# Optimization experiments

Measured on AMD Instinct MI355X. Metric: run time of the kernel, lower is better.

## Reference

```python
import jax, jax.numpy as jnp
import numpy as np

EPS_LN = 1e-5

def _layernorm(x, g, b):
    mu = jnp.mean(x, axis=-1, keepdims=True)
    var = jnp.mean((x - mu) ** 2, axis=-1, keepdims=True)
    return (x - mu) * jax.lax.rsqrt(var + EPS_LN) * g + b

def _act_quant_ste(x):
    # clip_val uses detached stats -> stop_gradient
    clip_val = jax.lax.stop_gradient(
        jnp.clip(jnp.mean(jnp.abs(x), axis=-1, keepdims=True), 1e-8, None)) * 2.5
    scale = clip_val / 127.0
    x_scaled = x / scale
    x_clip = jnp.clip(x_scaled, -127.0, 127.0)
    x_q = x_scaled + jax.lax.stop_gradient(jnp.round(x_clip) - x_scaled)
    return x_q * scale

def _weight_quant_ste(w):
    scale = jax.lax.stop_gradient(jnp.clip(jnp.mean(jnp.abs(w)), 1e-8, None))
    w_norm = w / scale
    w_clip = jnp.clip(w_norm, -1.0, 1.0)
    w_q = w_norm + jax.lax.stop_gradient(jnp.round(w_clip) - w_norm)
    return w_q * scale

def _bitlinear(x, w, g, b):
    # w: [out, in]; x: [B,T,in]
    x_q = _act_quant_ste(_layernorm(x, g, b))
    w_q = _weight_quant_ste(w)
    return jnp.einsum('btd,hd->bth', x_q, w_q)

def setup_inputs() -> dict:
    D, H = 2048, 2048 * 4
    B, T = 4, 2048
    key = jax.random.key(0)
    ks = jax.random.split(key, 4)
    std = 0.02
    return {
        'x': jax.random.normal(ks[0], (B, T, D), dtype=jnp.float32),
        'mu_k': jnp.zeros((1, 1, D), jnp.float32),
        'mu_r': jnp.zeros((1, 1, D), jnp.float32),
        'wk': jax.random.normal(ks[1], (H, D), jnp.float32) * std,
        'gk': jnp.ones((D,), jnp.float32), 'bk': jnp.zeros((D,), jnp.float32),
        'wr': jax.random.normal(ks[2], (D, D), jnp.float32) * std,
        'gr': jnp.ones((D,), jnp.float32), 'br': jnp.zeros((D,), jnp.float32),
        'wv': jax.random.normal(ks[3], (D, H), jnp.float32) * std,
        'gv': jnp.ones((H,), jnp.float32), 'bv': jnp.zeros((H,), jnp.float32),
    }

def reference(x, mu_k, mu_r, wk, gk, bk, wr, gr, br, wv, gv, bv):
    B, T, C = x.shape
    prev = jnp.zeros((B, 1, C), dtype=x.dtype)  # state=None path
    x_prev = jnp.concatenate([prev, x[:, :-1, :]], axis=1)  # token shift
    dx = x_prev - x
    k_act = jax.nn.relu(_bitlinear(x + dx * mu_k, wk, gk, bk)) ** 2  # [B,T,H]
    rgate = jax.nn.sigmoid(_bitlinear(x + dx * mu_r, wr, gr, br))    # [B,T,D]
    out = rgate * _bitlinear(k_act, wv, gv, bv)                      # [B,T,D]
    return out, jax.lax.stop_gradient(x[:, -1:, :])
```

## Files before the change

### kernel.cpp

```cpp
#include <hip/hip_runtime.h>

#define T_LEN 2048
#define B_SZ  4
#define D_DIM 2048
#define H_DIM 8192
#define BT    (B_SZ * T_LEN)

typedef float f32x4 __attribute__((ext_vector_type(4)));
typedef int   i32x4v __attribute__((ext_vector_type(4)));
typedef int   i32x16v __attribute__((ext_vector_type(16)));
typedef unsigned short ushort8 __attribute__((ext_vector_type(8)));

__device__ __forceinline__ float bf2f(unsigned short u) {
    unsigned int i = ((unsigned int)u) << 16;
    return __builtin_bit_cast(float, i);
}
__device__ __forceinline__ unsigned short f2bf(float f) {
    unsigned int i = __builtin_bit_cast(unsigned int, f);
    i += 0x7fffu + ((i >> 16) & 1u);
    return (unsigned short)(i >> 16);
}

__device__ __forceinline__ float block_sum(float v, float* red) {
    #pragma unroll
    for (int o = 32; o > 0; o >>= 1) v += __shfl_down(v, o, 64);
    const int lane = threadIdx.x & 63, w = threadIdx.x >> 6;
    if (lane == 0) red[w] = v;
    __syncthreads();
    float r = red[0] + red[1] + red[2] + red[3];
    __syncthreads();
    return r;
}

__global__ void wabs_all(const float* __restrict__ wk, const float* __restrict__ wr,
                         const float* __restrict__ wv, float* __restrict__ part) {
    __shared__ float red[16];
    const int m = blockIdx.x >> 10;
    const int blk = blockIdx.x & 1023;
    const float* w = (m == 0) ? wk : (m == 1) ? wr : wv;
    const int n = (m == 1) ? D_DIM * D_DIM : H_DIM * D_DIM;
    float s = 0.f;
    int i = (blk * 256 + threadIdx.x) * 8;
    const int stride = 1024 * 256 * 8;
    for (; i < n; i += stride) {
        f32x4 a = *(const f32x4*)(w + i);
        f32x4 b = *(const f32x4*)(w + i + 4);
        #pragma unroll
        for (int j = 0; j < 4; j++) s += fabsf(a[j]) + fabsf(b[j]);
    }
    float tot = block_sum(s, red);
    if (threadIdx.x == 0) part[blockIdx.x] = tot;
}

__global__ void wfinal_all(const float* __restrict__ part, float* __restrict__ wsc) {
    __shared__ float red[16];
    const int m = blockIdx.x;
    const int n = (m == 1) ? D_DIM * D_DIM : H_DIM * D_DIM;
    float s = 0.f;
    for (int i = threadIdx.x; i < 1024; i += 256) s += part[m * 1024 + i];
    float tot = block_sum(s, red);
    if (threadIdx.x == 0) wsc[m] = fmaxf(tot / (float)n, 1e-8f);
}

__global__ void wquant_all(const float* __restrict__ wk, const float* __restrict__ wr,
                           const float* __restrict__ wv,
                           signed char* __restrict__ qk, signed char* __restrict__ qr,
                           signed char* __restrict__ qv,
                           const float* __restrict__ wsc) {
    const int b = blockIdx.x;
    int m, blk, nblk;
    if (b < 2048)      { m = 0; blk = b;        nblk = 2048; }
    else if (b < 3072) { m = 1; blk = b - 2048; nblk = 1024; }
    else               { m = 2; blk = b - 3072; nblk = 2048; }
    const float* w = (m == 0) ? wk : (m == 1) ? wr : wv;
    signed char* q = (m == 0) ? qk : (m == 1) ? qr : qv;
    const int n = (m == 1) ? D_DIM * D_DIM : H_DIM * D_DIM;
    const float s = wsc[m];
    int i = (blk * 256 + threadIdx.x) * 16;
    const int stride = nblk * 256 * 16;
    for (; i < n; i += stride) {
        union { signed char c[16]; i32x4v v; } pk;
        #pragma unroll
        for (int h = 0; h < 4; h++) {
            f32x4 a = *(const f32x4*)(w + i + h * 4);
            #pragma unroll
            for (int j = 0; j < 4; j++)
                pk.c[h * 4 + j] =
                    (signed char)(int)rintf(fminf(fmaxf(a[j] / s, -1.f), 1.f));
        }
        *(i32x4v*)(q + i) = pk.v;
    }
}

__device__ __forceinline__ void ln_quant8(const float* xm_in,
                                          const float* __restrict__ g,
                                          const float* __restrict__ b,
                                          signed char* qbase, int row,
                                          float* srow, float* red) {
    const int base = threadIdx.x * 8;
    float xm[8];
    float s = 0.f;
    #pragma unroll
    for (int j = 0; j < 8; j++) { xm[j] = xm_in[j]; s += xm[j]; }
    const float mean = block_sum(s, red) * (1.f / D_DIM);
    float s2 = 0.f;
    #pragma unroll
    for (int j = 0; j < 8; j++) { float d = xm[j] - mean; s2 += d * d; }
    const float var  = block_sum(s2, red) * (1.f / D_DIM);
    const float rstd = 1.f / sqrtf(var + 1e-5f);
    f32x4 ga = *(const f32x4*)(g + base), gb = *(const f32x4*)(g + base + 4);
    f32x4 ba = *(const f32x4*)(b + base), bb2 = *(const f32x4*)(b + base + 4);
    float gg[8] = {ga[0],ga[1],ga[2],ga[3],gb[0],gb[1],gb[2],gb[3]};
    float bb[8] = {ba[0],ba[1],ba[2],ba[3],bb2[0],bb2[1],bb2[2],bb2[3]};
    float sa = 0.f;
    #pragma unroll
    for (int j = 0; j < 8; j++) {
        xm[j] = (xm[j] - mean) * rstd * gg[j] + bb[j];
        sa += fabsf(xm[j]);
    }
    const float amean = block_sum(sa, red) * (1.f / D_DIM);
    const float scale = fmaxf(amean, 1e-8f) * 2.5f / 127.0f;
    union { signed char c[8]; int2 v; } pk;
    #pragma unroll
    for (int j = 0; j < 8; j++)
        pk.c[j] = (signed char)(int)rintf(fminf(fmaxf(xm[j] / scale, -127.f), 127.f));
    const size_t addr = ((size_t)(row >> 5) * (D_DIM / 16) + (threadIdx.x >> 1)) * 512
                        + (row & 31) * 16 + (threadIdx.x & 1) * 8;
    *(int2*)(qbase + addr) = pk.v;
    if (threadIdx.x == 0) *srow = scale;
}

__global__ void act_prep(const float* __restrict__ x,
                         const float* __restrict__ muk,
                         const float* __restrict__ gk, const float* __restrict__ bk,
                         const float* __restrict__ mur,
                         const float* __restrict__ gr, const float* __restrict__ br,
                         signed char* __restrict__ qk, float* __restrict__ sk,
                         signed char* __restrict__ qr, float* __restrict__ sr,
                         float* __restrict__ out2) {
    __shared__ float red[16];
    const int row = blockIdx.x;
    const int t = row & (T_LEN - 1);
    const int base = threadIdx.x * 8;

    float xv[8], xp[8];
    f32x4 xa = *(const f32x4*)(x + (size_t)row * D_DIM + base);
    f32x4 xb = *(const f32x4*)(x + (size_t)row * D_DIM + base + 4);
    xv[0]=xa[0]; xv[1]=xa[1]; xv[2]=xa[2]; xv[3]=xa[3];
    xv[4]=xb[0]; xv[5]=xb[1]; xv[6]=xb[2]; xv[7]=xb[3];
    if (t > 0) {
        f32x4 pa = *(const f32x4*)(x + (size_t)(row - 1) * D_DIM + base);
        f32x4 pb = *(const f32x4*)(x + (size_t)(row - 1) * D_DIM + base + 4);
        xp[0]=pa[0]; xp[1]=pa[1]; xp[2]=pa[2]; xp[3]=pa[3];
        xp[4]=pb[0]; xp[5]=pb[1]; xp[6]=pb[2]; xp[7]=pb[3];
    } else {
        #pragma unroll
        for (int j = 0; j < 8; j++) xp[j] = 0.f;
    }
    if (t == T_LEN - 1) {
        const int bb = row / T_LEN;
        *(f32x4*)(out2 + (size_t)bb * D_DIM + base)     = xa;
        *(f32x4*)(out2 + (size_t)bb * D_DIM + base + 4) = xb;
    }
    float mk[8], mr[8], xmk[8], xmr[8];
    f32x4 mka = *(const f32x4*)(muk + base), mkb = *(const f32x4*)(muk + base + 4);
    f32x4 mra = *(const f32x4*)(mur + base), mrb = *(const f32x4*)(mur + base + 4);
    mk[0]=mka[0]; mk[1]=mka[1]; mk[2]=mka[2]; mk[3]=mka[3];
    mk[4]=mkb[0]; mk[5]=mkb[1]; mk[6]=mkb[2]; mk[7]=mkb[3];
    mr[0]=mra[0]; mr[1]=mra[1]; mr[2]=mra[2]; mr[3]=mra[3];
    mr[4]=mrb[0]; mr[5]=mrb[1]; mr[6]=mrb[2]; mr[7]=mrb[3];
    #pragma unroll
    for (int j = 0; j < 8; j++) {
        const float dx = xp[j] - xv[j];
        xmk[j] = xv[j] + dx * mk[j];
        xmr[j] = xv[j] + dx * mr[j];
    }
    ln_quant8(xmk, gk, bk, qk, row, sk + row, red);
    ln_quant8(xmr, gr, br, qr, row, sr + row, red);
}

__global__ void lnq_v(const unsigned short* __restrict__ kact,
                      const float* __restrict__ g, const float* __restrict__ b,
                      signed char* __restrict__ qv, float* __restrict__ sv) {
    __shared__ float red[16];
    const int row = blockIdx.x;
    const int base = threadIdx.x * 32;
    const unsigned short* kr = kact + (size_t)row * H_DIM + base;

    float v[32];
    float s = 0.f;
    #pragma unroll
    for (int c = 0; c < 4; c++) {
        ushort8 a = *(const ushort8*)(kr + c * 8);
        #pragma unroll
        for (int j = 0; j < 8; j++) { v[c * 8 + j] = bf2f(a[j]); s += v[c * 8 + j]; }
    }
    const float mean = block_sum(s, red) * (1.f / H_DIM);
    float s2 = 0.f;
    #pragma unroll
    for (int j = 0; j < 32; j++) { float d = v[j] - mean; s2 += d * d; }
    const float var  = block_sum(s2, red) * (1.f / H_DIM);
    const float rstd = 1.f / sqrtf(var + 1e-5f);
    float sa = 0.f;
    #pragma unroll
    for (int c = 0; c < 8; c++) {
        f32x4 ga = *(const f32x4*)(g + base + c * 4);
        f32x4 ba = *(const f32x4*)(b + base + c * 4);
        #pragma unroll
        for (int j = 0; j < 4; j++) {
            int k = c * 4 + j;
            v[k] = (v[k] - mean) * rstd * ga[j] + ba[j];
            sa += fabsf(v[k]);
        }
    }
    const float amean = block_sum(sa, red) * (1.f / H_DIM);
    const float scale = fmaxf(amean, 1e-8f) * 2.5f / 127.0f;
    union { signed char c[32]; i32x4v v4[2]; } pk;
    #pragma unroll
    for (int j = 0; j < 32; j++)
        pk.c[j] = (signed char)(int)rintf(fminf(fmaxf(v[j] / scale, -127.f), 127.f));
    const size_t tb = ((size_t)(row >> 5) * (H_DIM / 16) + threadIdx.x * 2) * 512
                      + (row & 31) * 16;
    *(i32x4v*)(qv + tb)       = pk.v4[0];
    *(i32x4v*)(qv + tb + 512) = pk.v4[1];
    if (threadIdx.x == 0) sv[row] = scale;
}

template <int EP>
__global__ __launch_bounds__(512, 2) void gemmP(
    const signed char* __restrict__ Ap, const signed char* __restrict__ B,
    int K, int Nn, int gn,
    const float* __restrict__ sa, const float* __restrict__ swp,
    const unsigned short* __restrict__ gate_bf, float* __restrict__ out_f,
    unsigned short* __restrict__ out_bf) {
    __shared__ signed char Bs[3 * 32768];
    const int tid = threadIdx.x;
    const int nwg = gridDim.x, q8 = nwg >> 3;
    const int swz = (blockIdx.x & 7) * q8 + (blockIdx.x >> 3);
    const int bm = swz / gn, bn = swz % gn;
    const int lane = tid & 63, wave = tid >> 6;
    const int lrow = lane & 31, lhalf = lane >> 5;
    const int KS = K >> 4;
    const size_t rts = (size_t)(bm * 8 + wave) * KS;
    const size_t brow0 = (size_t)bn * 128;
    const int NB = K >> 8;

    i32x16v acc[4] = {};

    auto stageB = [&](int p, int t) {
        const int r = tid >> 2, sl = tid & 3;
        #pragma unroll
        for (int j = 0; j < 4; j++) {
            const signed char* g = B + (brow0 + r) * (size_t)K + (t * 256 + j * 64)
                                   + ((sl ^ ((r >> 1) & 3)) * 16);
            __builtin_amdgcn_global_load_lds(
                (const __attribute__((address_space(1))) void*)g,
                (__attribute__((address_space(3))) void*)(Bs + p * 32768 + j * 8192 + tid * 16),
                16, 0, 0);
        }
    };
    auto loadA = [&](i32x4v (&a)[4][2], int t) {
        #pragma unroll
        for (int s = 0; s < 4; s++)
            #pragma unroll
            for (int sl = 0; sl < 2; sl++)
                a[s][sl] = *(const i32x4v*)(
                    Ap + ((rts + (size_t)(t * 16 + s * 4 + sl * 2)) << 9) + lane * 16);
    };
    auto readB = [&](int p, int s, i32x4v (&b)[4][2]) {
        const signed char* basep = Bs + p * 32768 + s * 8192;
        #pragma unroll
        for (int sl = 0; sl < 2; sl++) {
            const int slot = sl * 2 + lhalf;
            #pragma unroll
            for (int tn = 0; tn < 4; tn++) {
                const int r = tn * 32 + lrow;
                b[tn][sl] = *(const i32x4v*)(basep + r * 64 + ((slot ^ ((r >> 1) & 3)) * 16));
            }
        }
    };

    auto bodyf = [&](int t, i32x4v (&aC)[4][2], i32x4v (&aN)[4][2]) {
        const int p = t % 3;
        const bool pf = (t + 1 < NB);
        if (pf) {
            stageB((t + 1) % 3, t + 1);
            asm volatile("s_waitcnt vmcnt(12)" ::: "memory");
        } else {
            asm volatile("s_waitcnt vmcnt(8)" ::: "memory");
        }
        __builtin_amdgcn_sched_barrier(0);
        __builtin_amdgcn_s_barrier();
        __builtin_amdgcn_sched_barrier(0);
        if (pf) loadA(aN, t + 1);
        #pragma unroll
        for (int s = 0; s < 4; s++) {
            i32x4v b[4][2];
            readB(p, s, b);
            __builtin_amdgcn_s_setprio(1);
            #pragma unroll
            for (int sl = 0; sl < 2; sl++)
                #pragma unroll
                for (int tn = 0; tn < 4; tn++)
                    acc[tn] = __builtin_amdgcn_mfma_i32_32x32x32_i8(
                        aC[s][sl], b[tn][sl], acc[tn], 0, 0, 0);
            __builtin_amdgcn_s_setprio(0);
        }
    };

    i32x4v aE[4][2], aO[4][2];
    stageB(0, 0);
    loadA(aE, 0);
    for (int t = 0; t < NB; t += 2) {
        bodyf(t, aE, aO);
        bodyf(t + 1, aO, aE);
    }

    const float sw = *swp;
    #pragma unroll
    for (int tn = 0; tn < 4; tn++) {
        #pragma unroll
        for (int rg = 0; rg < 16; rg++) {
            const int rin  = (rg & 3) + 8 * (rg >> 2) + 4 * lhalf;
            const int grow = bm * 256 + wave * 32 + rin;
            const int gcol = bn * 128 + tn * 32 + lrow;
            const float v = (float)acc[tn][rg] * sa[grow] * sw;
            const size_t idx = (size_t)grow * Nn + gcol;
            if (EP == 0) {
                float rv = fmaxf(v, 0.f);
                out_bf[idx] = f2bf(rv * rv);
            } else if (EP == 1) {
                out_bf[idx] = f2bf(1.0f / (1.0f + expf(-v)));
            } else {
                out_f[idx] = bf2f(gate_bf[idx]) * v;
            }
        }
    }
}

extern "C" void kernel_launch(void* const* d_in, const int* in_sizes, int n_in,
                              void* d_out, int out_size, void* d_ws, size_t ws_size,
                              hipStream_t stream) {
    const float* x   = (const float*)d_in[0];
    const float* muk = (const float*)d_in[1];
    const float* mur = (const float*)d_in[2];
    const float* wk  = (const float*)d_in[3];
    const float* gk  = (const float*)d_in[4];
    const float* bk  = (const float*)d_in[5];
    const float* wr  = (const float*)d_in[6];
    const float* gr  = (const float*)d_in[7];
    const float* br  = (const float*)d_in[8];
    const float* wv  = (const float*)d_in[9];
    const float* gv  = (const float*)d_in[10];
    const float* bv  = (const float*)d_in[11];

    char* wsb = (char*)d_ws;
    size_t off = 0;
    auto alloc = [&](size_t bytes) -> size_t {
        size_t p = off;
        off = (off + bytes + 255) & ~(size_t)255;
        return p;
    };
    const size_t o_wqk  = alloc((size_t)H_DIM * D_DIM);
    const size_t o_wqr  = alloc((size_t)D_DIM * D_DIM);
    const size_t o_wqv  = alloc((size_t)D_DIM * H_DIM);
    const size_t o_wsc  = alloc(64);
    const size_t o_part = alloc(3 * 1024 * sizeof(float));
    const size_t o_xqk  = alloc((size_t)BT * D_DIM);
    const size_t o_xqr  = alloc((size_t)BT * D_DIM);
    const size_t o_gate = alloc((size_t)BT * D_DIM * 2);
    const size_t o_sk   = alloc((size_t)BT * 4);
    const size_t o_sr   = alloc((size_t)BT * 4);
    const size_t fixed  = off;

    int CH = BT;
    while (CH > 512 &&
           fixed + (size_t)CH * (H_DIM + 2 * H_DIM + 4) + 8192 > ws_size)
        CH >>= 1;
    const size_t o_xqv  = alloc((size_t)CH * H_DIM);
    const size_t o_kact = alloc((size_t)CH * H_DIM * 2);
    const size_t o_sv   = alloc((size_t)CH * 4);

    signed char* wqk = (signed char*)(wsb + o_wqk);
    signed char* wqr = (signed char*)(wsb + o_wqr);
    signed char* wqv = (signed char*)(wsb + o_wqv);
    float* wsc  = (float*)(wsb + o_wsc);
    float* part = (float*)(wsb + o_part);
    signed char* xqk = (signed char*)(wsb + o_xqk);
    signed char* xqr = (signed char*)(wsb + o_xqr);
    unsigned short* gate = (unsigned short*)(wsb + o_gate);
    float* sk = (float*)(wsb + o_sk);
    float* sr = (float*)(wsb + o_sr);
    signed char* xqv = (signed char*)(wsb + o_xqv);
    unsigned short* kact = (unsigned short*)(wsb + o_kact);
    float* sv = (float*)(wsb + o_sv);

    float* outp = (float*)d_out;
    float* out2 = outp + (size_t)BT * D_DIM;

    wabs_all<<<3072, 256, 0, stream>>>(wk, wr, wv, part);
    wfinal_all<<<3, 256, 0, stream>>>(part, wsc);
    wquant_all<<<5120, 256, 0, stream>>>(wk, wr, wv, wqk, wqr, wqv, wsc);

    act_prep<<<BT, 256, 0, stream>>>(x, muk, gk, bk, mur, gr, br,
                                     xqk, sk, xqr, sr, out2);

    gemmP<1><<<(BT / 256) * (D_DIM / 128), 512, 0, stream>>>(
        xqr, wqr, D_DIM, D_DIM, D_DIM / 128, sr, wsc + 1,
        (const unsigned short*)nullptr, (float*)nullptr, gate);

    for (int row0 = 0; row0 < BT; row0 += CH) {
        gemmP<0><<<(CH / 256) * (H_DIM / 128), 512, 0, stream>>>(
            xqk + (size_t)row0 * D_DIM, wqk, D_DIM, H_DIM, H_DIM / 128,
            sk + row0, wsc + 0,
            (const unsigned short*)nullptr, (float*)nullptr, kact);

        lnq_v<<<CH, 256, 0, stream>>>(kact, gv, bv, xqv, sv);

        gemmP<2><<<(CH / 256) * (D_DIM / 128), 512, 0, stream>>>(
            xqv, wqv, H_DIM, D_DIM, D_DIM / 128, sv, wsc + 2,
            gate + (size_t)row0 * D_DIM, outp + (size_t)row0 * D_DIM,
            (unsigned short*)nullptr);
    }
}
```

Measured before the change: 600.5 us.

## Reshape int8 GEMM tiles to 512x64 with 2x2 MFMA per wave

Changes the block tile from 256x128 to 512x64, so each wave computes a 64x64 output with a 2x2 grid of 32x32 MFMA tiles instead of 32x128. B staging in LDS is halved and each B fragment is reused across two A row tiles, lowering LDS read traffic per MFMA. B tiles are now prefetched two steps ahead with a tighter vmcnt wait. The cost is twice as many A register loads from global per wave, more registers held for A, and different occupancy and grid sizes.

Result: slower. 645.3 us (+7.5%).

```diff
diff --git a/kernel.cpp b/kernel.cpp
--- a/kernel.cpp
+++ b/kernel.cpp
@@ -227,13 +227,13 @@
 }
 
 template <int EP>
-__global__ __launch_bounds__(512, 2) void gemmP(
+__global__ __launch_bounds__(512, 2) void gemmQ(
     const signed char* __restrict__ Ap, const signed char* __restrict__ B,
     int K, int Nn, int gn,
     const float* __restrict__ sa, const float* __restrict__ swp,
     const unsigned short* __restrict__ gate_bf, float* __restrict__ out_f,
     unsigned short* __restrict__ out_bf) {
-    __shared__ signed char Bs[3 * 32768];
+    __shared__ signed char Bs[3][16384];
     const int tid = threadIdx.x;
     const int nwg = gridDim.x, q8 = nwg >> 3;
     const int swz = (blockIdx.x & 7) * q8 + (blockIdx.x >> 3);
@@ -241,76 +241,82 @@
     const int lane = tid & 63, wave = tid >> 6;
     const int lrow = lane & 31, lhalf = lane >> 5;
     const int KS = K >> 4;
-    const size_t rts = (size_t)(bm * 8 + wave) * KS;
-    const size_t brow0 = (size_t)bn * 128;
+    const size_t brow0 = (size_t)bn * 64;
     const int NB = K >> 8;
 
-    i32x16v acc[4] = {};
+    i32x16v acc[2][2] = {};
 
     auto stageB = [&](int p, int t) {
-        const int r = tid >> 2, sl = tid & 3;
-        #pragma unroll
-        for (int j = 0; j < 4; j++) {
-            const signed char* g = B + (brow0 + r) * (size_t)K + (t * 256 + j * 64)
+        #pragma unroll
+        for (int j = 0; j < 2; j++) {
+            const int o   = j * 512 + tid;
+            const int sub = o >> 8;
+            const int wi  = o & 255;
+            const int r   = wi >> 2;
+            const int sl  = wi & 3;
+            const signed char* g = B + (brow0 + r) * (size_t)K + t * 256 + sub * 64
                                    + ((sl ^ ((r >> 1) & 3)) * 16);
             __builtin_amdgcn_global_load_lds(
                 (const __attribute__((address_space(1))) void*)g,
-                (__attribute__((address_space(3))) void*)(Bs + p * 32768 + j * 8192 + tid * 16),
-                16, 0, 0);
+                (__attribute__((address_space(3))) void*)(&Bs[p][o * 16]), 16, 0, 0);
         }
     };
-    auto loadA = [&](i32x4v (&a)[4][2], int t) {
-        #pragma unroll
-        for (int s = 0; s < 4; s++)
+    auto loadA = [&](i32x4v (&a)[2][4][2], int t) {
+        #pragma unroll
+        for (int tm = 0; tm < 2; tm++) {
+            const size_t rt = (size_t)(bm * 16 + wave * 2 + tm) * KS;
+            const signed char* bp = Ap + ((rt + t * 16) << 9) + lane * 16;
             #pragma unroll
-            for (int sl = 0; sl < 2; sl++)
-                a[s][sl] = *(const i32x4v*)(
-                    Ap + ((rts + (size_t)(t * 16 + s * 4 + sl * 2)) << 9) + lane * 16);
+            for (int s = 0; s < 4; s++)
+                #pragma unroll
+                for (int sl = 0; sl < 2; sl++)
+                    a[tm][s][sl] = *(const i32x4v*)(bp + (size_t)(s * 4 + sl * 2) * 512);
+        }
     };
-    auto readB = [&](int p, int s, i32x4v (&b)[4][2]) {
-        const signed char* basep = Bs + p * 32768 + s * 8192;
+    auto readB = [&](int p, int s, i32x4v (&b)[2][2]) {
+        const signed char* basep = &Bs[p][s * 4096];
         #pragma unroll
         for (int sl = 0; sl < 2; sl++) {
             const int slot = sl * 2 + lhalf;
             #pragma unroll
-            for (int tn = 0; tn < 4; tn++) {
+            for (int tn = 0; tn < 2; tn++) {
                 const int r = tn * 32 + lrow;
                 b[tn][sl] = *(const i32x4v*)(basep + r * 64 + ((slot ^ ((r >> 1) & 3)) * 16));
             }
         }
     };
 
-    auto bodyf = [&](int t, i32x4v (&aC)[4][2], i32x4v (&aN)[4][2]) {
-        const int p = t % 3;
+    auto bodyf = [&](int t, i32x4v (&aC)[2][4][2], i32x4v (&aN)[2][4][2]) {
         const bool pf = (t + 1 < NB);
-        if (pf) {
-            stageB((t + 1) % 3, t + 1);
-            asm volatile("s_waitcnt vmcnt(12)" ::: "memory");
-        } else {
-            asm volatile("s_waitcnt vmcnt(8)" ::: "memory");
-        }
+        if (t > 0 && pf) stageB((t + 1) % 3, t + 1);
+        if (pf) asm volatile("s_waitcnt vmcnt(2)" ::: "memory");
+        else    asm volatile("s_waitcnt vmcnt(0)" ::: "memory");
         __builtin_amdgcn_sched_barrier(0);
         __builtin_amdgcn_s_barrier();
         __builtin_amdgcn_sched_barrier(0);
         if (pf) loadA(aN, t + 1);
+        const int p = t % 3;
         #pragma unroll
         for (int s = 0; s < 4; s++) {
-            i32x4v b[4][2];
+            i32x4v b[2][2];
             readB(p, s, b);
             __builtin_amdgcn_s_setprio(1);
             #pragma unroll
             for (int sl = 0; sl < 2; sl++)
                 #pragma unroll
-                for (int tn = 0; tn < 4; tn++)
-                    acc[tn] = __builtin_amdgcn_mfma_i32_32x32x32_i8(
-                        aC[s][sl], b[tn][sl], acc[tn], 0, 0, 0);
+                for (int tm = 0; tm < 2; tm++)
+                    #pragma unroll
+                    for (int tn = 0; tn < 2; tn++)
+                        acc[tm][tn] = __builtin_amdgcn_mfma_i32_32x32x32_i8(
+                            aC[tm][s][sl], b[tn][sl], acc[tm][tn], 0, 0, 0);
             __builtin_amdgcn_s_setprio(0);
         }
     };
 
-    i32x4v aE[4][2], aO[4][2];
+    i32x4v aE[2][4][2], aO[2][4][2];
     stageB(0, 0);
     loadA(aE, 0);
+    stageB(1, 1);
     for (int t = 0; t < NB; t += 2) {
         bodyf(t, aE, aO);
         bodyf(t + 1, aO, aE);
@@ -318,21 +324,24 @@
 
     const float sw = *swp;
     #pragma unroll
-    for (int tn = 0; tn < 4; tn++) {
-        #pragma unroll
-        for (int rg = 0; rg < 16; rg++) {
-            const int rin  = (rg & 3) + 8 * (rg >> 2) + 4 * lhalf;
-            const int grow = bm * 256 + wave * 32 + rin;
-            const int gcol = bn * 128 + tn * 32 + lrow;
-            const float v = (float)acc[tn][rg] * sa[grow] * sw;
-            const size_t idx = (size_t)grow * Nn + gcol;
-            if (EP == 0) {
-                float rv = fmaxf(v, 0.f);
-                out_bf[idx] = f2bf(rv * rv);
-            } else if (EP == 1) {
-                out_bf[idx] = f2bf(1.0f / (1.0f + expf(-v)));
-            } else {
-                out_f[idx] = bf2f(gate_bf[idx]) * v;
+    for (int tm = 0; tm < 2; tm++) {
+        #pragma unroll
+        for (int tn = 0; tn < 2; tn++) {
+            #pragma unroll
+            for (int rg = 0; rg < 16; rg++) {
+                const int rin  = (rg & 3) + 8 * (rg >> 2) + 4 * lhalf;
+                const int grow = bm * 512 + wave * 64 + tm * 32 + rin;
+                const int gcol = bn * 64 + tn * 32 + lrow;
+                const float v = (float)acc[tm][tn][rg] * sa[grow] * sw;
+                const size_t idx = (size_t)grow * Nn + gcol;
+                if (EP == 0) {
+                    float rv = fmaxf(v, 0.f);
+                    out_bf[idx] = f2bf(rv * rv);
+                } else if (EP == 1) {
+                    out_bf[idx] = f2bf(1.0f / (1.0f + expf(-v)));
+                } else {
+                    out_f[idx] = bf2f(gate_bf[idx]) * v;
+                }
             }
         }
     }
@@ -405,20 +414,20 @@
     act_prep<<<BT, 256, 0, stream>>>(x, muk, gk, bk, mur, gr, br,
                                      xqk, sk, xqr, sr, out2);
 
-    gemmP<1><<<(BT / 256) * (D_DIM / 128), 512, 0, stream>>>(
-        xqr, wqr, D_DIM, D_DIM, D_DIM / 128, sr, wsc + 1,
+    gemmQ<1><<<(BT / 512) * (D_DIM / 64), 512, 0, stream>>>(
+        xqr, wqr, D_DIM, D_DIM, D_DIM / 64, sr, wsc + 1,
         (const unsigned short*)nullptr, (float*)nullptr, gate);
 
     for (int row0 = 0; row0 < BT; row0 += CH) {
-        gemmP<0><<<(CH / 256) * (H_DIM / 128), 512, 0, stream>>>(
-            xqk + (size_t)row0 * D_DIM, wqk, D_DIM, H_DIM, H_DIM / 128,
+        gemmQ<0><<<(CH / 512) * (H_DIM / 64), 512, 0, stream>>>(
+            xqk + (size_t)row0 * D_DIM, wqk, D_DIM, H_DIM, H_DIM / 64,
             sk + row0, wsc + 0,
             (const unsigned short*)nullptr, (float*)nullptr, kact);
 
         lnq_v<<<CH, 256, 0, stream>>>(kact, gv, bv, xqv, sv);
 
-        gemmP<2><<<(CH / 256) * (D_DIM / 128), 512, 0, stream>>>(
-            xqv, wqv, H_DIM, D_DIM, D_DIM / 128, sv, wsc + 2,
+        gemmQ<2><<<(CH / 512) * (D_DIM / 64), 512, 0, stream>>>(
+            xqv, wqv, H_DIM, D_DIM, D_DIM / 64, sv, wsc + 2,
             gate + (size_t)row0 * D_DIM, outp + (size_t)row0 * D_DIM,
             (unsigned short*)nullptr);
     }
```

## Restructure int8 GEMM into 2x4 wave grid with finer K pipeline

Applied to the files above, without the earlier changes.

Replaces the int8 GEMM so the 8 waves form a 2x4 grid. Each wave now owns 128 rows by 32 columns, loads four A tiles from global memory and reads one B tile from LDS per sub-step, where before each wave took 32 rows across all 128 columns. The K step drops from 256 to 128, the LDS B buffer is halved to 3x16KB with a new XOR swizzle, and B is prefetched two steps ahead with split staging and barriers inside each phase. The goal is fewer LDS reads per MFMA and better overlap of global loads with compute. In exchange it adds more barriers per K step and twice as many A registers, which raises register pressure at launch bounds (512,2).

Measured after the change: 813.6 us. 1.35x slower.

```diff
diff --git a/kernel.cpp b/kernel.cpp
--- a/kernel.cpp
+++ b/kernel.cpp
@@ -227,104 +227,109 @@
 }
 
 template <int EP>
-__global__ __launch_bounds__(512, 2) void gemmP(
+__global__ __launch_bounds__(512, 2) void gemmF(
     const signed char* __restrict__ Ap, const signed char* __restrict__ B,
     int K, int Nn, int gn,
     const float* __restrict__ sa, const float* __restrict__ swp,
     const unsigned short* __restrict__ gate_bf, float* __restrict__ out_f,
     unsigned short* __restrict__ out_bf) {
-    __shared__ signed char Bs[3 * 32768];
+    __shared__ signed char Bs[3][16384];
     const int tid = threadIdx.x;
     const int nwg = gridDim.x, q8 = nwg >> 3;
     const int swz = (blockIdx.x & 7) * q8 + (blockIdx.x >> 3);
     const int bm = swz / gn, bn = swz % gn;
     const int lane = tid & 63, wave = tid >> 6;
+    const int wr = wave >> 2, wc = wave & 3;
     const int lrow = lane & 31, lhalf = lane >> 5;
     const int KS = K >> 4;
-    const size_t rts = (size_t)(bm * 8 + wave) * KS;
     const size_t brow0 = (size_t)bn * 128;
-    const int NB = K >> 8;
+    const int NB = K >> 7;
 
     i32x16v acc[4] = {};
 
-    auto stageB = [&](int p, int t) {
-        const int r = tid >> 2, sl = tid & 3;
-        #pragma unroll
-        for (int j = 0; j < 4; j++) {
-            const signed char* g = B + (brow0 + r) * (size_t)K + (t * 256 + j * 64)
-                                   + ((sl ^ ((r >> 1) & 3)) * 16);
-            __builtin_amdgcn_global_load_lds(
-                (const __attribute__((address_space(1))) void*)g,
-                (__attribute__((address_space(3))) void*)(Bs + p * 32768 + j * 8192 + tid * 16),
-                16, 0, 0);
-        }
+    auto stageB = [&](int p, int t, int j) {
+        const int o = j * 512 + tid;
+        const int r = o >> 3, sl = o & 7;
+        const signed char* g = B + (brow0 + r) * (size_t)K + t * 128
+                               + ((sl ^ (r & 7)) * 16);
+        __builtin_amdgcn_global_load_lds(
+            (const __attribute__((address_space(1))) void*)g,
+            (__attribute__((address_space(3))) void*)(&Bs[p][o * 16]), 16, 0, 0);
     };
-    auto loadA = [&](i32x4v (&a)[4][2], int t) {
-        #pragma unroll
-        for (int s = 0; s < 4; s++)
+    auto loadA = [&](i32x4v (&a)[4][2][2], int t) {
+        #pragma unroll
+        for (int tm = 0; tm < 4; tm++) {
+            const size_t rt = (size_t)(bm * 8 + wr * 4 + tm) * KS;
+            const signed char* bp = Ap + ((rt + (size_t)t * 8) << 9) + lane * 16;
             #pragma unroll
-            for (int sl = 0; sl < 2; sl++)
-                a[s][sl] = *(const i32x4v*)(
-                    Ap + ((rts + (size_t)(t * 16 + s * 4 + sl * 2)) << 9) + lane * 16);
+            for (int s = 0; s < 2; s++)
+                #pragma unroll
+                for (int sl = 0; sl < 2; sl++)
+                    a[tm][s][sl] = *(const i32x4v*)(bp + (size_t)(s * 4 + sl * 2) * 512);
+        }
     };
-    auto readB = [&](int p, int s, i32x4v (&b)[4][2]) {
-        const signed char* basep = Bs + p * 32768 + s * 8192;
+
+    auto phase = [&](int p, int s, i32x4v (&aC)[4][2][2]) {
+        i32x4v b[2];
+        const int r = wc * 32 + lrow;
         #pragma unroll
         for (int sl = 0; sl < 2; sl++) {
-            const int slot = sl * 2 + lhalf;
+            const int slot = s * 4 + sl * 2 + lhalf;
+            b[sl] = *(const i32x4v*)(&Bs[p][r * 128 + ((slot ^ (r & 7)) * 16)]);
+        }
+        __builtin_amdgcn_s_barrier();
+        asm volatile("s_waitcnt lgkmcnt(0)" ::: "memory");
+        __builtin_amdgcn_sched_barrier(0);
+        __builtin_amdgcn_s_setprio(1);
+        #pragma unroll
+        for (int sl = 0; sl < 2; sl++)
             #pragma unroll
-            for (int tn = 0; tn < 4; tn++) {
-                const int r = tn * 32 + lrow;
-                b[tn][sl] = *(const i32x4v*)(basep + r * 64 + ((slot ^ ((r >> 1) & 3)) * 16));
-            }
-        }
-    };
-
-    auto bodyf = [&](int t, i32x4v (&aC)[4][2], i32x4v (&aN)[4][2]) {
-        const int p = t % 3;
-        const bool pf = (t + 1 < NB);
-        if (pf) {
-            stageB((t + 1) % 3, t + 1);
-            asm volatile("s_waitcnt vmcnt(12)" ::: "memory");
-        } else {
-            asm volatile("s_waitcnt vmcnt(8)" ::: "memory");
-        }
+            for (int tm = 0; tm < 4; tm++)
+                acc[tm] = __builtin_amdgcn_mfma_i32_32x32x32_i8(
+                    aC[tm][s][sl], b[sl], acc[tm], 0, 0, 0);
+        __builtin_amdgcn_s_setprio(0);
         __builtin_amdgcn_sched_barrier(0);
         __builtin_amdgcn_s_barrier();
-        __builtin_amdgcn_sched_barrier(0);
-        if (pf) loadA(aN, t + 1);
-        #pragma unroll
-        for (int s = 0; s < 4; s++) {
-            i32x4v b[4][2];
-            readB(p, s, b);
-            __builtin_amdgcn_s_setprio(1);
-            #pragma unroll
-            for (int sl = 0; sl < 2; sl++)
-                #pragma unroll
-                for (int tn = 0; tn < 4; tn++)
-                    acc[tn] = __builtin_amdgcn_mfma_i32_32x32x32_i8(
-                        aC[s][sl], b[tn][sl], acc[tn], 0, 0, 0);
-            __builtin_amdgcn_s_setprio(0);
-        }
     };
 
-    i32x4v aE[4][2], aO[4][2];
-    stageB(0, 0);
+    i32x4v aE[4][2][2], aO[4][2][2];
+    stageB(0, 0, 0); stageB(0, 0, 1);
     loadA(aE, 0);
+    stageB(1, 1, 0); stageB(1, 1, 1);
+    asm volatile("s_waitcnt vmcnt(18)" ::: "memory");
+    __builtin_amdgcn_sched_barrier(0);
+    __builtin_amdgcn_s_barrier();
+
+    auto body = [&](int t, i32x4v (&aC)[4][2][2], i32x4v (&aN)[4][2][2]) {
+        const int p = t % 3;
+        const bool hasA = (t + 1 < NB);
+        const bool hasB = (t + 2 < NB);
+        if (hasA) loadA(aN, t + 1);
+        if (hasB) stageB((t + 2) % 3, t + 2, 0);
+        phase(p, 0, aC);
+        if (hasB) stageB((t + 2) % 3, t + 2, 1);
+        if (hasA) {
+            if (hasB) asm volatile("s_waitcnt vmcnt(18)" ::: "memory");
+            else      asm volatile("s_waitcnt vmcnt(16)" ::: "memory");
+            __builtin_amdgcn_sched_barrier(0);
+        }
+        phase(p, 1, aC);
+    };
+
     for (int t = 0; t < NB; t += 2) {
-        bodyf(t, aE, aO);
-        bodyf(t + 1, aO, aE);
+        body(t, aE, aO);
+        body(t + 1, aO, aE);
     }
 
     const float sw = *swp;
     #pragma unroll
-    for (int tn = 0; tn < 4; tn++) {
+    for (int tm = 0; tm < 4; tm++) {
         #pragma unroll
         for (int rg = 0; rg < 16; rg++) {
             const int rin  = (rg & 3) + 8 * (rg >> 2) + 4 * lhalf;
-            const int grow = bm * 256 + wave * 32 + rin;
-            const int gcol = bn * 128 + tn * 32 + lrow;
-            const float v = (float)acc[tn][rg] * sa[grow] * sw;
+            const int grow = bm * 256 + wr * 128 + tm * 32 + rin;
+            const int gcol = bn * 128 + wc * 32 + lrow;
+            const float v = (float)acc[tm][rg] * sa[grow] * sw;
             const size_t idx = (size_t)grow * Nn + gcol;
             if (EP == 0) {
                 float rv = fmaxf(v, 0.f);
@@ -405,19 +410,19 @@
     act_prep<<<BT, 256, 0, stream>>>(x, muk, gk, bk, mur, gr, br,
                                      xqk, sk, xqr, sr, out2);
 
-    gemmP<1><<<(BT / 256) * (D_DIM / 128), 512, 0, stream>>>(
+    gemmF<1><<<(BT / 256) * (D_DIM / 128), 512, 0, stream>>>(
         xqr, wqr, D_DIM, D_DIM, D_DIM / 128, sr, wsc + 1,
         (const unsigned short*)nullptr, (float*)nullptr, gate);
 
     for (int row0 = 0; row0 < BT; row0 += CH) {
-        gemmP<0><<<(CH / 256) * (H_DIM / 128), 512, 0, stream>>>(
+        gemmF<0><<<(CH / 256) * (H_DIM / 128), 512, 0, stream>>>(
             xqk + (size_t)row0 * D_DIM, wqk, D_DIM, H_DIM, H_DIM / 128,
             sk + row0, wsc + 0,
             (const unsigned short*)nullptr, (float*)nullptr, kact);
 
         lnq_v<<<CH, 256, 0, stream>>>(kact, gv, bv, xqv, sv);
 
-        gemmP<2><<<(CH / 256) * (D_DIM / 128), 512, 0, stream>>>(
+        gemmF<2><<<(CH / 256) * (D_DIM / 128), 512, 0, stream>>>(
             xqv, wqv, H_DIM, D_DIM, D_DIM / 128, sv, wsc + 2,
             gate + (size_t)row0 * D_DIM, outp + (size_t)row0 * D_DIM,
             (unsigned short*)nullptr);
```
